# Performance work log

Measured on AMD Instinct MI355X. Metric: run time of the kernel, lower is better.

Reference implementation:

```python
import jax, jax.numpy as jnp
import numpy as np

N_ATOMS = 300000
N_COLS = 8
VOCAB = 4096      # nn.Embedding(4096, per_col_dim)
D_COL = 32        # per_col_dim
HID = 256         # hidden_size
N_BONDS = 320000
B_GRAPHS = 6000
ATOMS_PER_GRAPH = 50
STEPS = 3
SENTINEL = 999999999


def _linear_params(key, fan_in, fan_out):
    lim = 1.0 / np.sqrt(fan_in)
    kw, kb = jax.random.split(key)
    W = jax.random.uniform(kw, (fan_out, fan_in), minval=-lim, maxval=lim, dtype=jnp.float32)
    b = jax.random.uniform(kb, (fan_out,), minval=-lim, maxval=lim, dtype=jnp.float32)
    return W, b


def setup_inputs() -> dict:
    key = jax.random.key(0)
    ks = jax.random.split(key, 8)
    a_features = jax.random.randint(ks[0], (N_ATOMS, N_COLS), 0, VOCAB, dtype=jnp.int32)
    uv = jax.random.randint(ks[1], (N_BONDS, 2), 0, N_ATOMS, dtype=jnp.int32)
    bextra = jax.random.randint(ks[2], (N_BONDS, 1), 0, 16, dtype=jnp.int32)
    b_features = jnp.concatenate([uv, bextra], axis=1)
    # contiguous equal-length scopes: graph i owns atoms [i*50, i*50+50)
    starts = np.arange(B_GRAPHS, dtype=np.int32) * ATOMS_PER_GRAPH
    lengths = np.full(B_GRAPHS, ATOMS_PER_GRAPH, dtype=np.int32)
    a_scopes = jnp.asarray(np.stack([starts, lengths], axis=1))
    emb_weights = jax.random.normal(ks[3], (N_COLS, VOCAB, D_COL), dtype=jnp.float32) * 0.02
    W_in, b_in = _linear_params(ks[4], D_COL, HID)
    W_self, b_self = _linear_params(ks[5], HID, HID)
    W_neigh, b_neigh = _linear_params(ks[6], HID, HID)
    W_out, b_out = _linear_params(ks[7], HID, HID)
    return {
        'a_features': a_features, 'b_features': b_features, 'a_scopes': a_scopes,
        'emb_weights': emb_weights,
        'W_in': W_in, 'b_in': b_in,
        'W_self': W_self, 'b_self': b_self,
        'W_neigh': W_neigh, 'b_neigh': b_neigh,
        'W_out': W_out, 'b_out': b_out,
    }


def reference(a_features, b_features, a_scopes, emb_weights,
              W_in, b_in, W_self, b_self, W_neigh, b_neigh, W_out, b_out):
    # --- per-column embedding lookup, summed over columns ---
    idx = jnp.remainder(a_features, VOCAB)
    idx = jnp.where(a_features >= SENTINEL, 0, idx)          # sentinel -> index 0
    x = jnp.zeros((a_features.shape[0], D_COL), dtype=emb_weights.dtype)
    for c in range(N_COLS):                                   # fixed small loop over columns
        x = x + emb_weights[c][idx[:, c]]
    h = x @ W_in.T + b_in                                     # [N, HID]
    # --- undirected edges -> two directed edge lists ---
    u = b_features[:, 0]
    v = b_features[:, 1]
    src = jnp.concatenate([u, v], axis=0)
    dst = jnp.concatenate([v, u], axis=0)
    # --- message passing steps ---
    for _ in range(STEPS):
        agg = jnp.zeros_like(h).at[dst].add(h[src])           # scatter-add neighbor sum
        h = jax.nn.relu(h @ W_self.T + b_self + agg @ W_neigh.T + b_neigh)
    h = h @ W_out.T + b_out
    # --- per-graph mean pooling over contiguous scopes ---
    lengths = a_scopes[:, 1]
    seg_ids = jnp.repeat(jnp.arange(a_scopes.shape[0]), lengths,
                         total_repeat_length=h.shape[0])
    sums = jax.ops.segment_sum(h, seg_ids, num_segments=a_scopes.shape[0])
    denom = jnp.maximum(lengths, 1).astype(h.dtype)[:, None]
    return sums / denom
```

## Files before the change

kernel.cpp:

```cpp
#include <hip/hip_runtime.h>

#define NATOMS 300000
#define NCOLS 8
#define VOCABSZ 4096
#define DCOL 32
#define HIDDIM 256
#define NBONDS 320000
#define NGRAPHS 6000
#define NSTEPS 3

constexpr int MP = 300032;
constexpr int MTILES128 = MP / 128;
constexpr int HSTR = 2 * HIDDIM;
constexpr int XSTR = 2 * DCOL;
constexpr int ECAP = 32;

typedef _Float16 f16;
typedef _Float16 f16x8 __attribute__((ext_vector_type(8)));
typedef float f32x4 __attribute__((ext_vector_type(4)));

constexpr float LO_SCALE = 2048.0f;
constexpr float INV_LO   = 1.0f / 2048.0f;

__device__ __forceinline__ void split2(float x, f16& h, f16& l) {
    h = (f16)x;
    l = (f16)((x - (float)h) * LO_SCALE);
}

__device__ __forceinline__ int swz(int row, int q) {
    return (row * 4 + (q ^ ((row >> 1) & 3))) * 8;
}

__device__ __forceinline__ void dma16(const f16* g, f16* l) {
    __builtin_amdgcn_global_load_lds(
        (const __attribute__((address_space(1))) uint32_t*)g,
        (__attribute__((address_space(3))) uint32_t*)l, 16, 0, 0);
}

static void* g_pool = nullptr;
__attribute__((constructor)) static void alloc_pool() {
    void* p = nullptr;
    if (hipMalloc(&p, (size_t)1024 * 1024 * 1024) == hipSuccess) {
        hipMemset(p, 0, (size_t)1024 * 1024 * 1024);
        g_pool = p;
    }
}

__global__ void fill_kernel(float* out, float v, int n) {
    int i = blockIdx.x * blockDim.x + threadIdx.x;
    if (i < n) out[i] = v;
}

__global__ void csr_build_kernel(const int* __restrict__ bf, int* __restrict__ cnt,
                                 int* __restrict__ csr) {
    int e = blockIdx.x * blockDim.x + threadIdx.x;
    if (e >= 2 * NBONDS) return;
    int src, dst;
    if (e < NBONDS) { src = bf[e * 3 + 0]; dst = bf[e * 3 + 1]; }
    else { int i = e - NBONDS; src = bf[i * 3 + 1]; dst = bf[i * 3 + 0]; }
    int slot = atomicAdd(&cnt[dst], 1);
    if (slot < ECAP) csr[dst * ECAP + slot] = src;
}

__global__ void wsplit_kernel(const float* __restrict__ W, f16* __restrict__ Wh,
                              f16* __restrict__ Wl, int n) {
    int i = blockIdx.x * blockDim.x + threadIdx.x;
    if (i >= n) return;
    split2(W[i], Wh[i], Wl[i]);
}

__global__ void bsum_kernel(const float* __restrict__ a, const float* __restrict__ b,
                            float* __restrict__ o) {
    int i = threadIdx.x;
    o[i] = a[i] + b[i];
}

__global__ void embed_kernel(const int* __restrict__ af, const float* __restrict__ emb,
                             f16* __restrict__ x) {
    int gid = blockIdx.x * blockDim.x + threadIdx.x;
    int i = gid >> 5, k = gid & 31;
    if (i >= NATOMS) return;
    float s = 0.0f;
#pragma unroll
    for (int c = 0; c < NCOLS; c++) {
        int v = af[i * NCOLS + c];
        int idx = v & (VOCABSZ - 1);
        if (v >= 999999999) idx = 0;
        s += emb[((size_t)c * VOCABSZ + idx) * DCOL + k];
    }
    f16 hi, lo;
    split2(s, hi, lo);
    x[(size_t)i * XSTR + k] = hi;
    x[(size_t)i * XSTR + DCOL + k] = lo;
}

__global__ void agg_kernel(const f16* __restrict__ H, f16* __restrict__ G,
                           const int* __restrict__ cnt, const int* __restrict__ csr) {
    int wid = (blockIdx.x * blockDim.x + threadIdx.x) >> 6;
    int lane = threadIdx.x & 63;
    if (wid >= NATOMS) return;
    float a0 = 0.f, a1 = 0.f, a2 = 0.f, a3 = 0.f,
          a4 = 0.f, a5 = 0.f, a6 = 0.f, a7 = 0.f;
    const int degr = cnt[wid];
    const int deg = degr < ECAP ? degr : ECAP;
    const int* eb = csr + (size_t)wid * ECAP;
    int j = 0;
    for (; j + 2 <= deg; j += 2) {
        const int2 ss = *(const int2*)(eb + j);
        const f16x8 v0 = *(const f16x8*)(H + (size_t)ss.x * HSTR + lane * 8);
        const f16x8 v1 = *(const f16x8*)(H + (size_t)ss.y * HSTR + lane * 8);
        a0 += (float)v0[0] + (float)v1[0];
        a1 += (float)v0[1] + (float)v1[1];
        a2 += (float)v0[2] + (float)v1[2];
        a3 += (float)v0[3] + (float)v1[3];
        a4 += (float)v0[4] + (float)v1[4];
        a5 += (float)v0[5] + (float)v1[5];
        a6 += (float)v0[6] + (float)v1[6];
        a7 += (float)v0[7] + (float)v1[7];
    }
    if (j < deg) {
        const int s0 = eb[j];
        const f16x8 v = *(const f16x8*)(H + (size_t)s0 * HSTR + lane * 8);
        a0 += (float)v[0]; a1 += (float)v[1]; a2 += (float)v[2]; a3 += (float)v[3];
        a4 += (float)v[4]; a5 += (float)v[5]; a6 += (float)v[6]; a7 += (float)v[7];
    }
    const bool isLo = lane >= 32;
    if (isLo) {
        a0 *= INV_LO; a1 *= INV_LO; a2 *= INV_LO; a3 *= INV_LO;
        a4 *= INV_LO; a5 *= INV_LO; a6 *= INV_LO; a7 *= INV_LO;
    }
    float s0 = a0 + __shfl_xor(a0, 32, 64);
    float s1 = a1 + __shfl_xor(a1, 32, 64);
    float s2 = a2 + __shfl_xor(a2, 32, 64);
    float s3 = a3 + __shfl_xor(a3, 32, 64);
    float s4 = a4 + __shfl_xor(a4, 32, 64);
    float s5 = a5 + __shfl_xor(a5, 32, 64);
    float s6 = a6 + __shfl_xor(a6, 32, 64);
    float s7 = a7 + __shfl_xor(a7, 32, 64);
    f16x8 o;
#define EMIT(J, S)                                                    \
    {                                                                 \
        const f16 hv = (f16)(S);                                      \
        o[J] = isLo ? (f16)(((S) - (float)hv) * LO_SCALE) : hv;       \
    }
    EMIT(0, s0) EMIT(1, s1) EMIT(2, s2) EMIT(3, s3)
    EMIT(4, s4) EMIT(5, s5) EMIT(6, s6) EMIT(7, s7)
#undef EMIT
    *(f16x8*)(G + (size_t)wid * HSTR + lane * 8) = o;
}

template <bool HAS_A2, bool RELU, int K>
__global__ __launch_bounds__(512, 2) void mfma_gemm(
    const f16* __restrict__ A1, const f16* __restrict__ A2,
    const f16* __restrict__ B1h, const f16* __restrict__ B1l,
    const f16* __restrict__ B2h, const f16* __restrict__ B2l,
    const float* __restrict__ bias, f16* __restrict__ C) {
    constexpr int OAH = 0, OAL = 4096, OBH = 8192, OBL = 16384, BUFH = 24576;
    __shared__ __align__(16) f16 lds[3 * BUFH];

    const int t = threadIdx.x;
    const int m0 = blockIdx.x * 128;
    const int lane = t & 63;
    const int wid = t >> 6;
    const int wr = wid >> 2;
    const int wc = wid & 3;
    const int quad = lane >> 4;
    const int l16 = lane & 15;

    const int ra_ = wid * 16 + (lane >> 2);
    const int qs_ = (lane & 3) ^ ((ra_ >> 1) & 3);
    const int ko_ = qs_ * 8;

    f32x4 acch[4][4], accl[4][4];
#pragma unroll
    for (int a = 0; a < 4; a++)
#pragma unroll
        for (int b = 0; b < 4; b++) {
            acch[a][b] = (f32x4){0.f, 0.f, 0.f, 0.f};
            accl[a][b] = (f32x4){0.f, 0.f, 0.f, 0.f};
        }

    constexpr int NMAT = HAS_A2 ? 2 : 1;
    constexpr int NST = (K / 32) * NMAT;

#define ISSUE_STAGE(S, BUF)                                                    \
    {                                                                          \
        const int mat_ = HAS_A2 ? ((S) & 1) : 0;                               \
        const int kb_ = (HAS_A2 ? ((S) >> 1) : (S)) * 32;                      \
        const f16* A_ = (mat_ == 0) ? A1 : A2;                                 \
        const f16* Bh_ = (mat_ == 0) ? B1h : B2h;                              \
        const f16* Bl_ = (mat_ == 0) ? B1l : B2l;                              \
        f16* const dst_ = lds + (BUF) * BUFH + wid * 512;                      \
        const size_t arow_ = (size_t)(m0 + ra_) * (2 * K) + kb_ + ko_;         \
        dma16(A_ + arow_, dst_ + OAH);                                         \
        dma16(A_ + arow_ + K, dst_ + OAL);                                     \
        const size_t brow_ = (size_t)ra_ * K + kb_ + ko_;                      \
        dma16(Bh_ + brow_, dst_ + OBH);                                        \
        dma16(Bh_ + brow_ + (size_t)128 * K, dst_ + OBH + 4096);               \
        dma16(Bl_ + brow_, dst_ + OBL);                                        \
        dma16(Bl_ + brow_ + (size_t)128 * K, dst_ + OBL + 4096);               \
    }

#define COMPUTE_STAGE(BUF)                                                     \
    {                                                                          \
        const f16* cb = lds + (BUF) * BUFH;                                    \
        const f16* sAh = cb + OAH;                                             \
        const f16* sAl = cb + OAL;                                             \
        const f16* sBh = cb + OBH;                                             \
        const f16* sBl = cb + OBL;                                             \
        f16x8 fah[4], fal[4];                                                  \
        _Pragma("unroll")                                                      \
        for (int mt = 0; mt < 4; mt++) {                                       \
            const int src = swz(wr * 64 + mt * 16 + l16, quad);                \
            fah[mt] = *(const f16x8*)(sAh + src);                              \
            fal[mt] = *(const f16x8*)(sAl + src);                              \
        }                                                                      \
        _Pragma("unroll")                                                      \
        for (int nt = 0; nt < 4; nt++) {                                       \
            const int src = swz(wc * 64 + nt * 16 + l16, quad);                \
            const f16x8 bh = *(const f16x8*)(sBh + src);                       \
            const f16x8 bl = *(const f16x8*)(sBl + src);                       \
            _Pragma("unroll")                                                  \
            for (int mt = 0; mt < 4; mt++) {                                   \
                acch[mt][nt] = __builtin_amdgcn_mfma_f32_16x16x32_f16(         \
                    fah[mt], bh, acch[mt][nt], 0, 0, 0);                       \
                accl[mt][nt] = __builtin_amdgcn_mfma_f32_16x16x32_f16(         \
                    fah[mt], bl, accl[mt][nt], 0, 0, 0);                       \
                accl[mt][nt] = __builtin_amdgcn_mfma_f32_16x16x32_f16(         \
                    fal[mt], bh, accl[mt][nt], 0, 0, 0);                       \
            }                                                                  \
        }                                                                      \
    }

    ISSUE_STAGE(0, 0);
    asm volatile("" ::: "memory");
    if (NST > 1) ISSUE_STAGE(1, 1);

    int buf = 0;
    for (int s = 0; s < NST - 1; s++) {
        asm volatile("s_waitcnt vmcnt(6) lgkmcnt(0)" ::: "memory");
        __builtin_amdgcn_s_barrier();
        __builtin_amdgcn_sched_barrier(0);
        if (s + 2 < NST) {
            int nb = buf + 2; if (nb >= 3) nb -= 3;
            ISSUE_STAGE(s + 2, nb);
        }
        COMPUTE_STAGE(buf);
        buf = (buf == 2) ? 0 : buf + 1;
    }
    asm volatile("s_waitcnt vmcnt(0) lgkmcnt(0)" ::: "memory");
    __builtin_amdgcn_s_barrier();
    __builtin_amdgcn_sched_barrier(0);
    COMPUTE_STAGE(buf);
#undef ISSUE_STAGE
#undef COMPUTE_STAGE

#pragma unroll
    for (int mt = 0; mt < 4; mt++) {
#pragma unroll
        for (int nt = 0; nt < 4; nt++) {
            const int col = wc * 64 + nt * 16 + l16;
            const float bv = bias[col];
#pragma unroll
            for (int r = 0; r < 4; r++) {
                const int row = m0 + wr * 64 + mt * 16 + quad * 4 + r;
                float v = acch[mt][nt][r] + accl[mt][nt][r] * INV_LO + bv;
                if (RELU) v = fmaxf(v, 0.f);
                f16 hi, lo;
                split2(v, hi, lo);
                C[(size_t)row * HSTR + col] = hi;
                C[(size_t)row * HSTR + HIDDIM + col] = lo;
            }
        }
    }
}

__global__ void readout_mean_kernel(const f16* __restrict__ H,
                                    const int* __restrict__ scopes, float* __restrict__ G) {
    int g = blockIdx.x;
    int n = threadIdx.x;
    int start = scopes[g * 2 + 0];
    int len = scopes[g * 2 + 1];
    float s = 0.f;
    for (int j = 0; j < len; j++) {
        const f16* row = H + (size_t)(start + j) * HSTR;
        s += (float)row[n] + (float)row[HIDDIM + n] * INV_LO;
    }
    int d = len > 1 ? len : 1;
    G[(size_t)g * HIDDIM + n] = s / (float)d;
}

__global__ __launch_bounds__(256) void out_gemm_kernel(
    const float* __restrict__ G, const float* __restrict__ W,
    const float* __restrict__ bias, float* __restrict__ out) {
    __shared__ float sG[16 * 256];
    const int g0 = blockIdx.x * 16;
    const int t = threadIdx.x;
#pragma unroll
    for (int i = 0; i < 16; i++) sG[i * 256 + t] = G[(size_t)(g0 + i) * 256 + t];
    __syncthreads();
    const float bv = bias[t];
    const float* wrow = W + (size_t)t * 256;
    float acc[16];
#pragma unroll
    for (int g = 0; g < 16; g++) acc[g] = 0.f;
    for (int k = 0; k < 256; k += 4) {
        const float4 w = *(const float4*)(wrow + k);
#pragma unroll
        for (int g = 0; g < 16; g++) {
            const float4 a = *(const float4*)(sG + g * 256 + k);
            acc[g] = fmaf(a.x, w.x, acc[g]);
            acc[g] = fmaf(a.y, w.y, acc[g]);
            acc[g] = fmaf(a.z, w.z, acc[g]);
            acc[g] = fmaf(a.w, w.w, acc[g]);
        }
    }
#pragma unroll
    for (int g = 0; g < 16; g++) out[(size_t)(g0 + g) * 256 + t] = acc[g] + bv;
}

extern "C" void kernel_launch(void* const* d_in, const int* in_sizes, int n_in,
                              void* d_out, int out_size, void* d_ws, size_t ws_size,
                              hipStream_t stream) {
    const int* a_features = (const int*)d_in[0];
    const int* b_features = (const int*)d_in[1];
    const int* a_scopes   = (const int*)d_in[2];
    const float* emb      = (const float*)d_in[3];
    const float* W_in     = (const float*)d_in[4];
    const float* b_in     = (const float*)d_in[5];
    const float* W_self   = (const float*)d_in[6];
    const float* b_self   = (const float*)d_in[7];
    const float* W_neigh  = (const float*)d_in[8];
    const float* b_neigh  = (const float*)d_in[9];
    const float* W_out    = (const float*)d_in[10];
    const float* b_out    = (const float*)d_in[11];

    if (g_pool == nullptr) {
        fill_kernel<<<(out_size + 255) / 256, 256, 0, stream>>>(
            (float*)d_out, 77777.0f, out_size);
        return;
    }

    f16* p = (f16*)g_pool;
    const size_t HB2 = (size_t)MP * HSTR;
    f16* bufA = p;
    f16* bufB = p + HB2;
    f16* bufC = p + 2 * HB2;
    f16* xbuf = p + 3 * HB2;
    f16* Winh = xbuf + (size_t)MP * XSTR;
    f16* Winl = Winh + HIDDIM * DCOL;
    f16* Wsh  = Winl + HIDDIM * DCOL;
    f16* Wsl  = Wsh + HIDDIM * HIDDIM;
    f16* Wnh  = Wsl + HIDDIM * HIDDIM;
    f16* Wnl  = Wnh + HIDDIM * HIDDIM;
    float* Gmean = (float*)(Wnl + HIDDIM * HIDDIM);
    float* bsum  = Gmean + (size_t)NGRAPHS * HIDDIM;
    int* csr = (int*)(bsum + HIDDIM);
    int* cnt = csr + (size_t)MP * ECAP;

    constexpr int NPAD = MP - NATOMS;

    hipMemsetAsync(cnt, 0, (size_t)MP * sizeof(int), stream);
    csr_build_kernel<<<(2 * NBONDS + 255) / 256, 256, 0, stream>>>(b_features, cnt, csr);
    wsplit_kernel<<<(HIDDIM * DCOL + 255) / 256, 256, 0, stream>>>(W_in, Winh, Winl, HIDDIM * DCOL);
    wsplit_kernel<<<(HIDDIM * HIDDIM + 255) / 256, 256, 0, stream>>>(W_self, Wsh, Wsl, HIDDIM * HIDDIM);
    wsplit_kernel<<<(HIDDIM * HIDDIM + 255) / 256, 256, 0, stream>>>(W_neigh, Wnh, Wnl, HIDDIM * HIDDIM);
    bsum_kernel<<<1, HIDDIM, 0, stream>>>(b_self, b_neigh, bsum);

    constexpr int PADH = NPAD * HSTR / 2;
    fill_kernel<<<(PADH + 255) / 256, 256, 0, stream>>>((float*)(bufA + (size_t)NATOMS * HSTR), 0.f, PADH);
    fill_kernel<<<(PADH + 255) / 256, 256, 0, stream>>>((float*)(bufB + (size_t)NATOMS * HSTR), 0.f, PADH);
    fill_kernel<<<(PADH + 255) / 256, 256, 0, stream>>>((float*)(bufC + (size_t)NATOMS * HSTR), 0.f, PADH);
    constexpr int PADX = NPAD * XSTR / 2;
    fill_kernel<<<(PADX + 255) / 256, 256, 0, stream>>>((float*)(xbuf + (size_t)NATOMS * XSTR), 0.f, PADX);

    embed_kernel<<<(NATOMS * DCOL + 255) / 256, 256, 0, stream>>>(a_features, emb, xbuf);
    mfma_gemm<false, false, DCOL><<<MTILES128, 512, 0, stream>>>(
        xbuf, nullptr, Winh, Winl, nullptr, nullptr, b_in, bufA);

    f16* h  = bufA;
    f16* g  = bufB;
    f16* hn = bufC;
    for (int s = 0; s < NSTEPS; s++) {
        agg_kernel<<<NATOMS / 4, 256, 0, stream>>>(h, g, cnt, csr);
        mfma_gemm<true, true, HIDDIM><<<MTILES128, 512, 0, stream>>>(
            h, g, Wsh, Wsl, Wnh, Wnl, bsum, hn);
        f16* old = h;
        h = hn; hn = g; g = old;
    }

    readout_mean_kernel<<<NGRAPHS, 256, 0, stream>>>(h, a_scopes, Gmean);
    out_gemm_kernel<<<NGRAPHS / 16, 256, 0, stream>>>(Gmean, W_out, b_out, (float*)d_out);
}
```

Before: 1.782 ms.

## Interleave LDS fragment loads and split prefetch into phased MFMA clusters with setprio

Restructures the GEMM main loop so each K-stage is split into four phases. Each phase issues a few LDS fragment reads and one chunk of the next-next stage's global-to-LDS DMA, then runs a cluster of MFMAs at raised wave priority between barriers. The aim is to overlap memory issue with matrix math and keep the MFMA pipe busy, in the style of ping-pong scheduling. The cost is extra barriers per stage, and the vmcnt accounting now depends on how the split chunks are ordered.

```diff
diff --git a/kernel.cpp b/kernel.cpp
--- a/kernel.cpp
+++ b/kernel.cpp
@@ -183,77 +183,140 @@
     constexpr int NMAT = HAS_A2 ? 2 : 1;
     constexpr int NST = (K / 32) * NMAT;
 
-#define ISSUE_STAGE(S, BUF)                                                    \
+#define CHUNK_A(S, BUF)                                                        \
     {                                                                          \
         const int mat_ = HAS_A2 ? ((S) & 1) : 0;                               \
         const int kb_ = (HAS_A2 ? ((S) >> 1) : (S)) * 32;                      \
         const f16* A_ = (mat_ == 0) ? A1 : A2;                                 \
-        const f16* Bh_ = (mat_ == 0) ? B1h : B2h;                              \
-        const f16* Bl_ = (mat_ == 0) ? B1l : B2l;                              \
         f16* const dst_ = lds + (BUF) * BUFH + wid * 512;                      \
         const size_t arow_ = (size_t)(m0 + ra_) * (2 * K) + kb_ + ko_;         \
         dma16(A_ + arow_, dst_ + OAH);                                         \
         dma16(A_ + arow_ + K, dst_ + OAL);                                     \
+    }
+#define CHUNK_BH(S, BUF)                                                       \
+    {                                                                          \
+        const int mat_ = HAS_A2 ? ((S) & 1) : 0;                               \
+        const int kb_ = (HAS_A2 ? ((S) >> 1) : (S)) * 32;                      \
+        const f16* Bh_ = (mat_ == 0) ? B1h : B2h;                              \
+        f16* const dst_ = lds + (BUF) * BUFH + wid * 512;                      \
         const size_t brow_ = (size_t)ra_ * K + kb_ + ko_;                      \
         dma16(Bh_ + brow_, dst_ + OBH);                                        \
         dma16(Bh_ + brow_ + (size_t)128 * K, dst_ + OBH + 4096);               \
+    }
+#define CHUNK_BL(S, BUF)                                                       \
+    {                                                                          \
+        const int mat_ = HAS_A2 ? ((S) & 1) : 0;                               \
+        const int kb_ = (HAS_A2 ? ((S) >> 1) : (S)) * 32;                      \
+        const f16* Bl_ = (mat_ == 0) ? B1l : B2l;                              \
+        f16* const dst_ = lds + (BUF) * BUFH + wid * 512;                      \
+        const size_t brow_ = (size_t)ra_ * K + kb_ + ko_;                      \
         dma16(Bl_ + brow_, dst_ + OBL);                                        \
         dma16(Bl_ + brow_ + (size_t)128 * K, dst_ + OBL + 4096);               \
     }
 
-#define COMPUTE_STAGE(BUF)                                                     \
-    {                                                                          \
-        const f16* cb = lds + (BUF) * BUFH;                                    \
-        const f16* sAh = cb + OAH;                                             \
-        const f16* sAl = cb + OAL;                                             \
-        const f16* sBh = cb + OBH;                                             \
-        const f16* sBl = cb + OBL;                                             \
-        f16x8 fah[4], fal[4];                                                  \
-        _Pragma("unroll")                                                      \
-        for (int mt = 0; mt < 4; mt++) {                                       \
-            const int src = swz(wr * 64 + mt * 16 + l16, quad);                \
-            fah[mt] = *(const f16x8*)(sAh + src);                              \
-            fal[mt] = *(const f16x8*)(sAl + src);                              \
-        }                                                                      \
-        _Pragma("unroll")                                                      \
-        for (int nt = 0; nt < 4; nt++) {                                       \
-            const int src = swz(wc * 64 + nt * 16 + l16, quad);                \
-            const f16x8 bh = *(const f16x8*)(sBh + src);                       \
-            const f16x8 bl = *(const f16x8*)(sBl + src);                       \
-            _Pragma("unroll")                                                  \
-            for (int mt = 0; mt < 4; mt++) {                                   \
-                acch[mt][nt] = __builtin_amdgcn_mfma_f32_16x16x32_f16(         \
-                    fah[mt], bh, acch[mt][nt], 0, 0, 0);                       \
-                accl[mt][nt] = __builtin_amdgcn_mfma_f32_16x16x32_f16(         \
-                    fah[mt], bl, accl[mt][nt], 0, 0, 0);                       \
-                accl[mt][nt] = __builtin_amdgcn_mfma_f32_16x16x32_f16(         \
-                    fal[mt], bh, accl[mt][nt], 0, 0, 0);                       \
-            }                                                                  \
-        }                                                                      \
-    }
-
-    ISSUE_STAGE(0, 0);
+#define PHASE_OPEN()                                                           \
+    __builtin_amdgcn_s_barrier();                                              \
+    asm volatile("s_waitcnt lgkmcnt(0)" ::: "memory");                         \
+    __builtin_amdgcn_sched_barrier(0);                                         \
+    __builtin_amdgcn_s_setprio(1)
+#define PHASE_CLOSE()                                                          \
+    __builtin_amdgcn_s_setprio(0);                                             \
+    __builtin_amdgcn_sched_barrier(0);                                         \
+    __builtin_amdgcn_s_barrier()
+
+#define MFMA(D, X, Y) D = __builtin_amdgcn_mfma_f32_16x16x32_f16(X, Y, D, 0, 0, 0)
+
+    CHUNK_A(0, 0); CHUNK_BH(0, 0); CHUNK_BL(0, 0);
     asm volatile("" ::: "memory");
-    if (NST > 1) ISSUE_STAGE(1, 1);
+    if (NST > 1) { CHUNK_A(1, 1); CHUNK_BH(1, 1); CHUNK_BL(1, 1); }
+    if (NST > 1) { asm volatile("s_waitcnt vmcnt(6)" ::: "memory"); }
+    else         { asm volatile("s_waitcnt vmcnt(0)" ::: "memory"); }
+    __builtin_amdgcn_s_barrier();
+    __builtin_amdgcn_sched_barrier(0);
 
     int buf = 0;
-    for (int s = 0; s < NST - 1; s++) {
-        asm volatile("s_waitcnt vmcnt(6) lgkmcnt(0)" ::: "memory");
+    for (int s = 0; s < NST; s++) {
+        const bool pf = (s + 2 < NST);
+        int nb = buf + 2; if (nb >= 3) nb -= 3;
+        const f16* cb = lds + buf * BUFH;
+        const f16* sAh = cb + OAH;
+        const f16* sAl = cb + OAL;
+        const f16* sBh = cb + OBH;
+        const f16* sBl = cb + OBL;
+        f16x8 fah[4], fal[4], bh[4], bl[4];
+        const int ar0 = swz(wr * 64 + 0 * 16 + l16, quad);
+        const int ar1 = swz(wr * 64 + 1 * 16 + l16, quad);
+        const int ar2 = swz(wr * 64 + 2 * 16 + l16, quad);
+        const int ar3 = swz(wr * 64 + 3 * 16 + l16, quad);
+        const int br0 = swz(wc * 64 + 0 * 16 + l16, quad);
+        const int br1 = swz(wc * 64 + 1 * 16 + l16, quad);
+        const int br2 = swz(wc * 64 + 2 * 16 + l16, quad);
+        const int br3 = swz(wc * 64 + 3 * 16 + l16, quad);
+
+        fah[0] = *(const f16x8*)(sAh + ar0);
+        fah[1] = *(const f16x8*)(sAh + ar1);
+        fah[2] = *(const f16x8*)(sAh + ar2);
+        fah[3] = *(const f16x8*)(sAh + ar3);
+        bh[0]  = *(const f16x8*)(sBh + br0);
+        bh[1]  = *(const f16x8*)(sBh + br1);
+        if (pf) CHUNK_A(s + 2, nb);
+        PHASE_OPEN();
+#pragma unroll
+        for (int mt = 0; mt < 4; mt++) MFMA(acch[mt][0], fah[mt], bh[0]);
+#pragma unroll
+        for (int mt = 0; mt < 4; mt++) MFMA(acch[mt][1], fah[mt], bh[1]);
+        PHASE_CLOSE();
+
+        bh[2] = *(const f16x8*)(sBh + br2);
+        bh[3] = *(const f16x8*)(sBh + br3);
+        bl[0] = *(const f16x8*)(sBl + br0);
+        bl[1] = *(const f16x8*)(sBl + br1);
+        if (pf) CHUNK_BH(s + 2, nb);
+        PHASE_OPEN();
+#pragma unroll
+        for (int mt = 0; mt < 4; mt++) MFMA(acch[mt][2], fah[mt], bh[2]);
+#pragma unroll
+        for (int mt = 0; mt < 4; mt++) MFMA(acch[mt][3], fah[mt], bh[3]);
+        PHASE_CLOSE();
+
+        bl[2]  = *(const f16x8*)(sBl + br2);
+        bl[3]  = *(const f16x8*)(sBl + br3);
+        fal[0] = *(const f16x8*)(sAl + ar0);
+        fal[1] = *(const f16x8*)(sAl + ar1);
+        if (pf) CHUNK_BL(s + 2, nb);
+        PHASE_OPEN();
+#pragma unroll
+        for (int mt = 0; mt < 4; mt++) MFMA(accl[mt][0], fah[mt], bl[0]);
+#pragma unroll
+        for (int mt = 0; mt < 4; mt++) MFMA(accl[mt][1], fah[mt], bl[1]);
+        PHASE_CLOSE();
+
+        fal[2] = *(const f16x8*)(sAl + ar2);
+        fal[3] = *(const f16x8*)(sAl + ar3);
+        PHASE_OPEN();
+#pragma unroll
+        for (int mt = 0; mt < 4; mt++) MFMA(accl[mt][2], fah[mt], bl[2]);
+#pragma unroll
+        for (int mt = 0; mt < 4; mt++) MFMA(accl[mt][3], fah[mt], bl[3]);
+#pragma unroll
+        for (int nt = 0; nt < 4; nt++)
+#pragma unroll
+            for (int mt = 0; mt < 4; mt++) MFMA(accl[mt][nt], fal[mt], bh[nt]);
+        __builtin_amdgcn_s_setprio(0);
+        __builtin_amdgcn_sched_barrier(0);
+        if (s < NST - 2) { asm volatile("s_waitcnt vmcnt(6)" ::: "memory"); }
+        else             { asm volatile("s_waitcnt vmcnt(0)" ::: "memory"); }
         __builtin_amdgcn_s_barrier();
         __builtin_amdgcn_sched_barrier(0);
-        if (s + 2 < NST) {
-            int nb = buf + 2; if (nb >= 3) nb -= 3;
-            ISSUE_STAGE(s + 2, nb);
-        }
-        COMPUTE_STAGE(buf);
+
         buf = (buf == 2) ? 0 : buf + 1;
     }
-    asm volatile("s_waitcnt vmcnt(0) lgkmcnt(0)" ::: "memory");
-    __builtin_amdgcn_s_barrier();
-    __builtin_amdgcn_sched_barrier(0);
-    COMPUTE_STAGE(buf);
-#undef ISSUE_STAGE
-#undef COMPUTE_STAGE
+#undef CHUNK_A
+#undef CHUNK_BH
+#undef CHUNK_BL
+#undef PHASE_OPEN
+#undef PHASE_CLOSE
+#undef MFMA
 
 #pragma unroll
     for (int mt = 0; mt < 4; mt++) {
```

After: 1.862 ms. 1.04x slower.

## Use 256-row tiles with 32x32x16 MFMA and single accumulator split-precision GEMM

Applied to the files above, without the earlier changes.

The split-fp16 GEMM now processes 256-row tiles instead of 128 and switches from 16x16x32 to 32x32x16 MFMA instructions. The separate hi and lo accumulators are folded into one by pre-scaling the hi operands by 1/64, with the lo scale dropped from 2048 to 64. The LDS staging is restructured into separate ring buffers per operand with a different issue and wait schedule. The aim is more reuse of each B tile, fewer LDS reads per MFMA and lower accumulator register pressure. The lower lo scale risks losing precision, and the pipeline needs more LDS.

```diff
diff --git a/kernel.cpp b/kernel.cpp
--- a/kernel.cpp
+++ b/kernel.cpp
@@ -10,25 +10,21 @@
 #define NSTEPS 3
 
 constexpr int MP = 300032;
-constexpr int MTILES128 = MP / 128;
+constexpr int MTILES256 = MP / 256;
 constexpr int HSTR = 2 * HIDDIM;
 constexpr int XSTR = 2 * DCOL;
 constexpr int ECAP = 32;
 
 typedef _Float16 f16;
 typedef _Float16 f16x8 __attribute__((ext_vector_type(8)));
-typedef float f32x4 __attribute__((ext_vector_type(4)));
-
-constexpr float LO_SCALE = 2048.0f;
-constexpr float INV_LO   = 1.0f / 2048.0f;
+typedef float f32x16 __attribute__((ext_vector_type(16)));
+
+constexpr float LO_SCALE = 64.0f;
+constexpr float INV_LO   = 1.0f / 64.0f;
 
 __device__ __forceinline__ void split2(float x, f16& h, f16& l) {
     h = (f16)x;
     l = (f16)((x - (float)h) * LO_SCALE);
-}
-
-__device__ __forceinline__ int swz(int row, int q) {
-    return (row * 4 + (q ^ ((row >> 1) & 3))) * 8;
 }
 
 __device__ __forceinline__ void dma16(const f16* g, f16* l) {
@@ -155,116 +151,151 @@
     const f16* __restrict__ B1h, const f16* __restrict__ B1l,
     const f16* __restrict__ B2h, const f16* __restrict__ B2l,
     const float* __restrict__ bias, f16* __restrict__ C) {
-    constexpr int OAH = 0, OAL = 4096, OBH = 8192, OBL = 16384, BUFH = 24576;
-    __shared__ __align__(16) f16 lds[3 * BUFH];
+    constexpr int HB = 8192;
+    __shared__ __align__(16) f16 lds[9 * HB];
 
     const int t = threadIdx.x;
-    const int m0 = blockIdx.x * 128;
+    const int m0 = blockIdx.x * 256;
     const int lane = t & 63;
     const int wid = t >> 6;
-    const int wr = wid >> 2;
-    const int wc = wid & 3;
-    const int quad = lane >> 4;
-    const int l16 = lane & 15;
-
-    const int ra_ = wid * 16 + (lane >> 2);
-    const int qs_ = (lane & 3) ^ ((ra_ >> 1) & 3);
-    const int ko_ = qs_ * 8;
-
-    f32x4 acch[4][4], accl[4][4];
-#pragma unroll
-    for (int a = 0; a < 4; a++)
-#pragma unroll
-        for (int b = 0; b < 4; b++) {
-            acch[a][b] = (f32x4){0.f, 0.f, 0.f, 0.f};
-            accl[a][b] = (f32x4){0.f, 0.f, 0.f, 0.f};
-        }
+    const int wr = wid >> 1;
+    const int wc = wid & 1;
+    const int l31 = lane & 31;
+    const int kg = lane >> 5;
+
+    const int srow = wid * 16 + (lane >> 2);
+    const int sko = ((lane & 3) ^ (srow & 3)) * 8;
+
+    f32x16 acc[2][4];
+#pragma unroll
+    for (int a = 0; a < 2; a++)
+#pragma unroll
+        for (int b = 0; b < 4; b++)
+#pragma unroll
+            for (int i = 0; i < 16; i++) acc[a][b][i] = 0.f;
 
     constexpr int NMAT = HAS_A2 ? 2 : 1;
     constexpr int NST = (K / 32) * NMAT;
 
-#define ISSUE_STAGE(S, BUF)                                                    \
+#define SRC_DECL(S)                                                            \
+    const int mat_ = HAS_A2 ? ((S) & 1) : 0;                                   \
+    const int kb_ = (HAS_A2 ? ((S) >> 1) : (S)) * 32;
+
+#define ISSUE_AH(S)                                                            \
     {                                                                          \
-        const int mat_ = HAS_A2 ? ((S) & 1) : 0;                               \
-        const int kb_ = (HAS_A2 ? ((S) >> 1) : (S)) * 32;                      \
+        SRC_DECL(S)                                                            \
         const f16* A_ = (mat_ == 0) ? A1 : A2;                                 \
-        const f16* Bh_ = (mat_ == 0) ? B1h : B2h;                              \
-        const f16* Bl_ = (mat_ == 0) ? B1l : B2l;                              \
-        f16* const dst_ = lds + (BUF) * BUFH + wid * 512;                      \
-        const size_t arow_ = (size_t)(m0 + ra_) * (2 * K) + kb_ + ko_;         \
-        dma16(A_ + arow_, dst_ + OAH);                                         \
-        dma16(A_ + arow_ + K, dst_ + OAL);                                     \
-        const size_t brow_ = (size_t)ra_ * K + kb_ + ko_;                      \
-        dma16(Bh_ + brow_, dst_ + OBH);                                        \
-        dma16(Bh_ + brow_ + (size_t)128 * K, dst_ + OBH + 4096);               \
-        dma16(Bl_ + brow_, dst_ + OBL);                                        \
-        dma16(Bl_ + brow_ + (size_t)128 * K, dst_ + OBL + 4096);               \
-    }
-
-#define COMPUTE_STAGE(BUF)                                                     \
+        f16* dst_ = lds + ((S) % 3) * HB + wid * 512;                          \
+        dma16(A_ + (size_t)(m0 + srow) * (2 * K) + kb_ + sko, dst_);           \
+        dma16(A_ + (size_t)(m0 + srow + 128) * (2 * K) + kb_ + sko, dst_ + 4096); \
+    }
+#define ISSUE_AL(S)                                                            \
     {                                                                          \
-        const f16* cb = lds + (BUF) * BUFH;                                    \
-        const f16* sAh = cb + OAH;                                             \
-        const f16* sAl = cb + OAL;                                             \
-        const f16* sBh = cb + OBH;                                             \
-        const f16* sBl = cb + OBL;                                             \
-        f16x8 fah[4], fal[4];                                                  \
-        _Pragma("unroll")                                                      \
-        for (int mt = 0; mt < 4; mt++) {                                       \
-            const int src = swz(wr * 64 + mt * 16 + l16, quad);                \
-            fah[mt] = *(const f16x8*)(sAh + src);                              \
-            fal[mt] = *(const f16x8*)(sAl + src);                              \
-        }                                                                      \
-        _Pragma("unroll")                                                      \
-        for (int nt = 0; nt < 4; nt++) {                                       \
-            const int src = swz(wc * 64 + nt * 16 + l16, quad);                \
-            const f16x8 bh = *(const f16x8*)(sBh + src);                       \
-            const f16x8 bl = *(const f16x8*)(sBl + src);                       \
-            _Pragma("unroll")                                                  \
-            for (int mt = 0; mt < 4; mt++) {                                   \
-                acch[mt][nt] = __builtin_amdgcn_mfma_f32_16x16x32_f16(         \
-                    fah[mt], bh, acch[mt][nt], 0, 0, 0);                       \
-                accl[mt][nt] = __builtin_amdgcn_mfma_f32_16x16x32_f16(         \
-                    fah[mt], bl, accl[mt][nt], 0, 0, 0);                       \
-                accl[mt][nt] = __builtin_amdgcn_mfma_f32_16x16x32_f16(         \
-                    fal[mt], bh, accl[mt][nt], 0, 0, 0);                       \
-            }                                                                  \
-        }                                                                      \
-    }
-
-    ISSUE_STAGE(0, 0);
-    asm volatile("" ::: "memory");
-    if (NST > 1) ISSUE_STAGE(1, 1);
-
-    int buf = 0;
-    for (int s = 0; s < NST - 1; s++) {
-        asm volatile("s_waitcnt vmcnt(6) lgkmcnt(0)" ::: "memory");
-        __builtin_amdgcn_s_barrier();
-        __builtin_amdgcn_sched_barrier(0);
-        if (s + 2 < NST) {
-            int nb = buf + 2; if (nb >= 3) nb -= 3;
-            ISSUE_STAGE(s + 2, nb);
-        }
-        COMPUTE_STAGE(buf);
-        buf = (buf == 2) ? 0 : buf + 1;
-    }
-    asm volatile("s_waitcnt vmcnt(0) lgkmcnt(0)" ::: "memory");
+        SRC_DECL(S)                                                            \
+        const f16* A_ = (mat_ == 0) ? A1 : A2;                                 \
+        f16* dst_ = lds + (3 + ((S) & 1)) * HB + wid * 512;                    \
+        dma16(A_ + (size_t)(m0 + srow) * (2 * K) + K + kb_ + sko, dst_);       \
+        dma16(A_ + (size_t)(m0 + srow + 128) * (2 * K) + K + kb_ + sko, dst_ + 4096); \
+    }
+#define ISSUE_BH(S)                                                            \
+    {                                                                          \
+        SRC_DECL(S)                                                            \
+        const f16* B_ = (mat_ == 0) ? B1h : B2h;                               \
+        f16* dst_ = lds + (5 + ((S) & 1)) * HB + wid * 512;                    \
+        dma16(B_ + (size_t)srow * K + kb_ + sko, dst_);                        \
+        dma16(B_ + (size_t)(srow + 128) * K + kb_ + sko, dst_ + 4096);         \
+    }
+#define ISSUE_BL(S)                                                            \
+    {                                                                          \
+        SRC_DECL(S)                                                            \
+        const f16* B_ = (mat_ == 0) ? B1l : B2l;                               \
+        f16* dst_ = lds + (7 + ((S) & 1)) * HB + wid * 512;                    \
+        dma16(B_ + (size_t)srow * K + kb_ + sko, dst_);                        \
+        dma16(B_ + (size_t)(srow + 128) * K + kb_ + sko, dst_ + 4096);         \
+    }
+
+#define MFMA32(D, X, Y) D = __builtin_amdgcn_mfma_f32_32x32x16_f16(X, Y, D, 0, 0, 0)
+
+    ISSUE_AH(0);
+    ISSUE_AL(0);
+    ISSUE_BH(0);
+    ISSUE_BL(0);
+    if (NST > 1) {
+        ISSUE_AH(1);
+        asm volatile("s_waitcnt vmcnt(2)" ::: "memory");
+    } else {
+        asm volatile("s_waitcnt vmcnt(0)" ::: "memory");
+    }
     __builtin_amdgcn_s_barrier();
     __builtin_amdgcn_sched_barrier(0);
-    COMPUTE_STAGE(buf);
-#undef ISSUE_STAGE
-#undef COMPUTE_STAGE
-
-#pragma unroll
-    for (int mt = 0; mt < 4; mt++) {
+
+    for (int s = 0; s < NST; s++) {
+        if (s + 1 < NST) { ISSUE_AL(s + 1); ISSUE_BH(s + 1); ISSUE_BL(s + 1); }
+        if (s + 2 < NST) { ISSUE_AH(s + 2); }
+
+        const f16* pAH = lds + (s % 3) * HB;
+        const f16* pAL = lds + (3 + (s & 1)) * HB;
+        const f16* pBH = lds + (5 + (s & 1)) * HB;
+        const f16* pBL = lds + (7 + (s & 1)) * HB;
+
+#pragma unroll
+        for (int ks = 0; ks < 2; ks++) {
+            f16x8 ah[2], ahq[2], al[2], bh[4], bhq[4], bl[4];
+#pragma unroll
+            for (int mt = 0; mt < 2; mt++) {
+                const int r = wr * 64 + mt * 32 + l31;
+                const int ad = r * 32 + ((((ks << 1) | kg) ^ (r & 3)) << 3);
+                ah[mt] = *(const f16x8*)(pAH + ad);
+                al[mt] = *(const f16x8*)(pAL + ad);
+                ahq[mt] = ah[mt] * (f16)INV_LO;
+            }
+#pragma unroll
+            for (int nt = 0; nt < 4; nt++) {
+                const int r = wc * 128 + nt * 32 + l31;
+                const int ad = r * 32 + ((((ks << 1) | kg) ^ (r & 3)) << 3);
+                bh[nt] = *(const f16x8*)(pBH + ad);
+                bl[nt] = *(const f16x8*)(pBL + ad);
+                bhq[nt] = bh[nt] * (f16)INV_LO;
+            }
+#pragma unroll
+            for (int nt = 0; nt < 4; nt++)
+#pragma unroll
+                for (int mt = 0; mt < 2; mt++) MFMA32(acc[mt][nt], ah[mt], bh[nt]);
+#pragma unroll
+            for (int nt = 0; nt < 4; nt++)
+#pragma unroll
+                for (int mt = 0; mt < 2; mt++) MFMA32(acc[mt][nt], ahq[mt], bl[nt]);
+#pragma unroll
+            for (int nt = 0; nt < 4; nt++)
+#pragma unroll
+                for (int mt = 0; mt < 2; mt++) MFMA32(acc[mt][nt], al[mt], bhq[nt]);
+        }
+
+        if (s + 1 < NST) {
+            asm volatile("s_waitcnt lgkmcnt(0)" ::: "memory");
+            if (s + 2 < NST) { asm volatile("s_waitcnt vmcnt(2)" ::: "memory"); }
+            else             { asm volatile("s_waitcnt vmcnt(0)" ::: "memory"); }
+            __builtin_amdgcn_s_barrier();
+            __builtin_amdgcn_sched_barrier(0);
+        }
+    }
+#undef SRC_DECL
+#undef ISSUE_AH
+#undef ISSUE_AL
+#undef ISSUE_BH
+#undef ISSUE_BL
+#undef MFMA32
+
+#pragma unroll
+    for (int mt = 0; mt < 2; mt++) {
 #pragma unroll
         for (int nt = 0; nt < 4; nt++) {
-            const int col = wc * 64 + nt * 16 + l16;
+            const int col = wc * 128 + nt * 32 + l31;
             const float bv = bias[col];
 #pragma unroll
-            for (int r = 0; r < 4; r++) {
-                const int row = m0 + wr * 64 + mt * 16 + quad * 4 + r;
-                float v = acch[mt][nt][r] + accl[mt][nt][r] * INV_LO + bv;
+            for (int reg = 0; reg < 16; reg++) {
+                const int row = m0 + wr * 64 + mt * 32 + 4 * kg + (reg & 3) + 8 * (reg >> 2);
+                float v = acc[mt][nt][reg] + bv;
                 if (RELU) v = fmaxf(v, 0.f);
                 f16 hi, lo;
                 split2(v, hi, lo);
@@ -375,7 +406,7 @@
     fill_kernel<<<(PADX + 255) / 256, 256, 0, stream>>>((float*)(xbuf + (size_t)NATOMS * XSTR), 0.f, PADX);
 
     embed_kernel<<<(NATOMS * DCOL + 255) / 256, 256, 0, stream>>>(a_features, emb, xbuf);
-    mfma_gemm<false, false, DCOL><<<MTILES128, 512, 0, stream>>>(
+    mfma_gemm<false, false, DCOL><<<MTILES256, 512, 0, stream>>>(
         xbuf, nullptr, Winh, Winl, nullptr, nullptr, b_in, bufA);
 
     f16* h  = bufA;
@@ -383,7 +414,7 @@
     f16* hn = bufC;
     for (int s = 0; s < NSTEPS; s++) {
         agg_kernel<<<NATOMS / 4, 256, 0, stream>>>(h, g, cnt, csr);
-        mfma_gemm<true, true, HIDDIM><<<MTILES128, 512, 0, stream>>>(
+        mfma_gemm<true, true, HIDDIM><<<MTILES256, 512, 0, stream>>>(
             h, g, Wsh, Wsl, Wnh, Wnl, bsum, hn);
         f16* old = h;
         h = hn; hn = g; g = old;
```

After: 1.843 ms. 1.03x slower.
